# Kernel tuning notes

Measured on AMD Instinct MI355X. Metric: run time of the kernel, lower is better.

Reference implementation:

```python
import jax, jax.numpy as jnp
import numpy as np

EPS = 1e-6
CLASS_LAMBDA = 1.0
BBOX_LAMBDA = 1.0
IOU_LAMBDA = 1.0

B, Q, C1, T = 8, 900, 92, 1600  # batch, queries, num_classes+1, total targets


def _make_boxes(u):
    # turn uniform [.,4] noise into valid xyxy boxes in [0,1]
    xy = u[..., :2] * 0.7
    wh = u[..., 2:] * 0.3 + 0.01
    return jnp.concatenate([xy, xy + wh], axis=-1)


def setup_inputs() -> dict:
    key = jax.random.key(0)
    k1, k2, k3, k4 = jax.random.split(key, 4)
    pred_logits = jax.random.normal(k1, (B, Q, C1), dtype=jnp.float32)
    pred_bbox = _make_boxes(jax.random.uniform(k2, (B, Q, 4), dtype=jnp.float32))
    tgt_ids = jax.random.randint(k3, (T,), 0, 91, dtype=jnp.int32)
    tgt_bbox = _make_boxes(jax.random.uniform(k4, (T, 4), dtype=jnp.float32))
    return {"pred_logits": pred_logits, "pred_bbox": pred_bbox,
            "tgt_ids": tgt_ids, "tgt_bbox": tgt_bbox}


def _ciou_pairwise(b1, b2):
    # b1: [M,4], b2: [N,4] xyxy -> CIoU [M,N]
    b1 = b1[:, None, :]
    b2 = b2[None, :, :]
    x1 = jnp.maximum(b1[..., 0], b2[..., 0])
    y1 = jnp.maximum(b1[..., 1], b2[..., 1])
    x2 = jnp.minimum(b1[..., 2], b2[..., 2])
    y2 = jnp.minimum(b1[..., 3], b2[..., 3])
    inter = jnp.clip(x2 - x1, 0.0) * jnp.clip(y2 - y1, 0.0)
    w1 = b1[..., 2] - b1[..., 0]
    h1 = b1[..., 3] - b1[..., 1]
    w2 = b2[..., 2] - b2[..., 0]
    h2 = b2[..., 3] - b2[..., 1]
    union = w1 * h1 + w2 * h2 - inter
    iou = inter / (union + EPS)
    cw = jnp.maximum(b1[..., 2], b2[..., 2]) - jnp.minimum(b1[..., 0], b2[..., 0])
    ch = jnp.maximum(b1[..., 3], b2[..., 3]) - jnp.minimum(b1[..., 1], b2[..., 1])
    convex_diag_sq = cw ** 2 + ch ** 2
    center_dist_sq = ((b2[..., 0] + b2[..., 2] - b1[..., 0] - b1[..., 2]) ** 2
                      + (b2[..., 1] + b2[..., 3] - b1[..., 1] - b1[..., 3]) ** 2)
    dist_penalty = center_dist_sq / (convex_diag_sq + EPS) / 4.0
    v = (4.0 / jnp.pi ** 2) * (jnp.arctan(w2 / (h2 + EPS)) - jnp.arctan(w1 / (h1 + EPS))) ** 2
    alpha = jax.lax.stop_gradient(v / (1.0 + EPS - iou + v))  # torch no_grad
    return iou - dist_penalty - alpha * v


def reference(pred_logits, pred_bbox, tgt_ids, tgt_bbox):
    bsz, nq = pred_logits.shape[:2]
    out_prob = jax.nn.softmax(pred_logits.reshape(bsz * nq, -1), axis=-1)  # [BQ, C+1]
    out_bbox = pred_bbox.reshape(bsz * nq, 4)                              # [BQ, 4]
    cost_class = -out_prob[:, tgt_ids]                                     # [BQ, T]
    # L1 cdist
    cost_bbox = jnp.sum(jnp.abs(out_bbox[:, None, :] - tgt_bbox[None, :, :]), axis=-1)
    cost_iou = -_ciou_pairwise(out_bbox, tgt_bbox)                         # [BQ, T]
    cost = BBOX_LAMBDA * cost_bbox + CLASS_LAMBDA * cost_class + IOU_LAMBDA * cost_iou
    return cost.reshape(bsz, nq, -1)  # [B, Q, T]
```

## Files before the change

kernel.cpp:

```cpp
#include <hip/hip_runtime.h>
#include <math.h>

#define EPSF 1e-6f

constexpr int B_ = 8, Q_ = 900, C1_ = 92, T_ = 1600;
constexpr int NROW = B_ * Q_;
constexpr int PSTRIDE = 96;
constexpr int RPB = 16;
constexpr int TPB = 320;

__global__ __launch_bounds__(64) void precompute_kernel(
    const float* __restrict__ logits,
    const float* __restrict__ pbox,
    const float* __restrict__ tbox,
    float* __restrict__ probs,
    float* __restrict__ predd,
    float* __restrict__ tgtd)
{
    const int bid  = blockIdx.x;
    const int lane = threadIdx.x;

    if (bid < NROW) {
        const float* lrow = logits + (size_t)bid * C1_;
        float x0 = -INFINITY, x1 = -INFINITY;
        if (lane < C1_)      x0 = lrow[lane];
        if (lane + 64 < C1_) x1 = lrow[lane + 64];
        float m = fmaxf(x0, x1);
        #pragma unroll
        for (int off = 32; off; off >>= 1) m = fmaxf(m, __shfl_xor(m, off));
        float e0 = (lane < C1_)      ? __expf(x0 - m) : 0.0f;
        float e1 = (lane + 64 < C1_) ? __expf(x1 - m) : 0.0f;
        float s = e0 + e1;
        #pragma unroll
        for (int off = 32; off; off >>= 1) s += __shfl_xor(s, off);
        const float inv = 1.0f / s;
        float* prow = probs + (size_t)bid * PSTRIDE;
        if (lane < C1_)      prow[lane]      = e0 * inv;
        if (lane + 64 < C1_) prow[lane + 64] = e1 * inv;

        if (lane == 0) {
            const float bx1 = pbox[bid * 4 + 0];
            const float by1 = pbox[bid * 4 + 1];
            const float bx2 = pbox[bid * 4 + 2];
            const float by2 = pbox[bid * 4 + 3];
            const float w = bx2 - bx1, h = by2 - by1;
            float* d = predd + bid * 8;
            d[0] = bx1; d[1] = by1; d[2] = bx2; d[3] = by2;
            d[4] = w * h;
            d[5] = atanf(w / (h + EPSF));
            d[6] = bx1 + bx2;
            d[7] = by1 + by2;
        }
    } else {
        const int t = (bid - NROW) * 64 + lane;
        if (t < T_) {
            const float bx1 = tbox[t * 4 + 0];
            const float by1 = tbox[t * 4 + 1];
            const float bx2 = tbox[t * 4 + 2];
            const float by2 = tbox[t * 4 + 3];
            const float w = bx2 - bx1, h = by2 - by1;
            float* d = tgtd + t * 8;
            d[0] = bx1; d[1] = by1; d[2] = bx2; d[3] = by2;
            d[4] = w * h;
            d[5] = atanf(w / (h + EPSF));
            d[6] = bx1 + bx2;
            d[7] = by1 + by2;
        }
    }
}

__global__ __launch_bounds__(TPB) void cost_kernel(
    const float* __restrict__ probs,
    const float* __restrict__ predd,
    const float* __restrict__ tgtd,
    const int*   __restrict__ ids,
    float* __restrict__ out)
{
    __shared__ float sprobs[RPB * PSTRIDE];
    __shared__ float spredd[RPB * 8];

    const int tid  = threadIdx.x;
    const int t    = blockIdx.x * TPB + tid;
    const int row0 = blockIdx.y * RPB;

    {
        const float4* gp4 = (const float4*)(probs + (size_t)row0 * PSTRIDE);
        float4* sp4 = (float4*)sprobs;
        sp4[tid] = gp4[tid];
        if (tid < RPB * PSTRIDE / 4 - TPB)
            sp4[tid + TPB] = gp4[tid + TPB];
        const float4* gd4 = (const float4*)(predd + (size_t)row0 * 8);
        float4* sd4 = (float4*)spredd;
        if (tid < RPB * 8 / 4)
            sd4[tid] = gd4[tid];
    }

    const float4 ta = *(const float4*)(tgtd + (size_t)t * 8);
    const float4 tb = *(const float4*)(tgtd + (size_t)t * 8 + 4);
    const int id = ids[t];
    const float tx1 = ta.x, ty1 = ta.y, tx2 = ta.z, ty2 = ta.w;
    const float area2 = tb.x, atan2t = tb.y, sx2 = tb.z, sy2 = tb.w;

    __syncthreads();

    float* outp = out + (size_t)row0 * T_ + t;
    #pragma unroll 4
    for (int r = 0; r < RPB; ++r) {
        const float4 pa = *(const float4*)(spredd + r * 8);
        const float4 pb = *(const float4*)(spredd + r * 8 + 4);
        const float px1 = pa.x, py1 = pa.y, px2 = pa.z, py2 = pa.w;
        const float area1 = pb.x, atan1t = pb.y, sx1 = pb.z, sy1 = pb.w;

        const float prob = sprobs[r * PSTRIDE + id];

        const float ix1 = fmaxf(px1, tx1);
        const float iy1 = fmaxf(py1, ty1);
        const float ix2 = fminf(px2, tx2);
        const float iy2 = fminf(py2, ty2);
        const float inter = fmaxf(ix2 - ix1, 0.0f) * fmaxf(iy2 - iy1, 0.0f);
        const float uni = area1 + area2 - inter;
        const float iou = inter * __builtin_amdgcn_rcpf(uni + EPSF);

        const float cw = fmaxf(px2, tx2) - fminf(px1, tx1);
        const float ch = fmaxf(py2, ty2) - fminf(py1, ty1);
        const float diag = cw * cw + ch * ch;
        const float dx = sx2 - sx1, dy = sy2 - sy1;
        const float cdist = dx * dx + dy * dy;
        const float dist_pen = cdist * __builtin_amdgcn_rcpf(diag + EPSF) * 0.25f;

        const float dat = atan2t - atan1t;
        const float v = (4.0f / (float)(M_PI * M_PI)) * dat * dat;
        const float av = v * v * __builtin_amdgcn_rcpf(1.0f + EPSF - iou + v);

        const float ciou = iou - dist_pen - av;

        const float cost_bbox = fabsf(px1 - tx1) + fabsf(py1 - ty1) +
                                fabsf(px2 - tx2) + fabsf(py2 - ty2);

        __builtin_nontemporal_store(cost_bbox - prob - ciou, outp);
        outp += T_;
    }
}

extern "C" void kernel_launch(void* const* d_in, const int* in_sizes, int n_in,
                              void* d_out, int out_size, void* d_ws, size_t ws_size,
                              hipStream_t stream) {
    const float* logits = (const float*)d_in[0];
    const float* pbox   = (const float*)d_in[1];
    const int*   ids    = (const int*)d_in[2];
    const float* tbox   = (const float*)d_in[3];
    float* out = (float*)d_out;

    float* ws    = (float*)d_ws;
    float* probs = ws;
    float* predd = probs + (size_t)NROW * PSTRIDE;
    float* tgtd  = predd + (size_t)NROW * 8;

    const int nTgtBlocks = (T_ + 63) / 64;
    precompute_kernel<<<NROW + nTgtBlocks, 64, 0, stream>>>(
        logits, pbox, tbox, probs, predd, tgtd);

    cost_kernel<<<dim3(T_ / TPB, NROW / RPB), TPB, 0, stream>>>(
        probs, predd, tgtd, ids, out);
}
```

Baseline: 96.03 us.

## Fuse softmax and box precompute into the cost kernel, dropping the precompute launch

Removes the separate precompute kernel. Each cost block now loads its 16 raw logit rows into shared memory and runs the softmax there with per-wave shuffle reductions, computes the predicted-box derived values in shared memory, and computes target-box derived values, including the atan, per thread. This cuts a kernel launch and the workspace round trip through global memory. In exchange the softmax is recomputed once per column block (5x redundant), an extra barrier is added, and each thread evaluates an atan.

```diff
diff --git a/kernel.cpp b/kernel.cpp
--- a/kernel.cpp
+++ b/kernel.cpp
@@ -5,78 +5,18 @@
 
 constexpr int B_ = 8, Q_ = 900, C1_ = 92, T_ = 1600;
 constexpr int NROW = B_ * Q_;
-constexpr int PSTRIDE = 96;
 constexpr int RPB = 16;
 constexpr int TPB = 320;
+constexpr int LSTRIDE = 92;
 
-__global__ __launch_bounds__(64) void precompute_kernel(
+__global__ __launch_bounds__(TPB) void fused_cost_kernel(
     const float* __restrict__ logits,
     const float* __restrict__ pbox,
+    const int*   __restrict__ ids,
     const float* __restrict__ tbox,
-    float* __restrict__ probs,
-    float* __restrict__ predd,
-    float* __restrict__ tgtd)
-{
-    const int bid  = blockIdx.x;
-    const int lane = threadIdx.x;
-
-    if (bid < NROW) {
-        const float* lrow = logits + (size_t)bid * C1_;
-        float x0 = -INFINITY, x1 = -INFINITY;
-        if (lane < C1_)      x0 = lrow[lane];
-        if (lane + 64 < C1_) x1 = lrow[lane + 64];
-        float m = fmaxf(x0, x1);
-        #pragma unroll
-        for (int off = 32; off; off >>= 1) m = fmaxf(m, __shfl_xor(m, off));
-        float e0 = (lane < C1_)      ? __expf(x0 - m) : 0.0f;
-        float e1 = (lane + 64 < C1_) ? __expf(x1 - m) : 0.0f;
-        float s = e0 + e1;
-        #pragma unroll
-        for (int off = 32; off; off >>= 1) s += __shfl_xor(s, off);
-        const float inv = 1.0f / s;
-        float* prow = probs + (size_t)bid * PSTRIDE;
-        if (lane < C1_)      prow[lane]      = e0 * inv;
-        if (lane + 64 < C1_) prow[lane + 64] = e1 * inv;
-
-        if (lane == 0) {
-            const float bx1 = pbox[bid * 4 + 0];
-            const float by1 = pbox[bid * 4 + 1];
-            const float bx2 = pbox[bid * 4 + 2];
-            const float by2 = pbox[bid * 4 + 3];
-            const float w = bx2 - bx1, h = by2 - by1;
-            float* d = predd + bid * 8;
-            d[0] = bx1; d[1] = by1; d[2] = bx2; d[3] = by2;
-            d[4] = w * h;
-            d[5] = atanf(w / (h + EPSF));
-            d[6] = bx1 + bx2;
-            d[7] = by1 + by2;
-        }
-    } else {
-        const int t = (bid - NROW) * 64 + lane;
-        if (t < T_) {
-            const float bx1 = tbox[t * 4 + 0];
-            const float by1 = tbox[t * 4 + 1];
-            const float bx2 = tbox[t * 4 + 2];
-            const float by2 = tbox[t * 4 + 3];
-            const float w = bx2 - bx1, h = by2 - by1;
-            float* d = tgtd + t * 8;
-            d[0] = bx1; d[1] = by1; d[2] = bx2; d[3] = by2;
-            d[4] = w * h;
-            d[5] = atanf(w / (h + EPSF));
-            d[6] = bx1 + bx2;
-            d[7] = by1 + by2;
-        }
-    }
-}
-
-__global__ __launch_bounds__(TPB) void cost_kernel(
-    const float* __restrict__ probs,
-    const float* __restrict__ predd,
-    const float* __restrict__ tgtd,
-    const int*   __restrict__ ids,
     float* __restrict__ out)
 {
-    __shared__ float sprobs[RPB * PSTRIDE];
+    __shared__ float sprobs[RPB * LSTRIDE];
     __shared__ float spredd[RPB * 8];
 
     const int tid  = threadIdx.x;
@@ -84,22 +24,54 @@
     const int row0 = blockIdx.y * RPB;
 
     {
-        const float4* gp4 = (const float4*)(probs + (size_t)row0 * PSTRIDE);
-        float4* sp4 = (float4*)sprobs;
-        sp4[tid] = gp4[tid];
-        if (tid < RPB * PSTRIDE / 4 - TPB)
-            sp4[tid + TPB] = gp4[tid + TPB];
-        const float4* gd4 = (const float4*)(predd + (size_t)row0 * 8);
-        float4* sd4 = (float4*)spredd;
-        if (tid < RPB * 8 / 4)
-            sd4[tid] = gd4[tid];
+        const float4* gl4 = (const float4*)(logits + (size_t)row0 * C1_);
+        float4* sl4 = (float4*)sprobs;
+        sl4[tid] = gl4[tid];
+        if (tid < RPB * C1_ / 4 - TPB)
+            sl4[tid + TPB] = gl4[tid + TPB];
     }
 
-    const float4 ta = *(const float4*)(tgtd + (size_t)t * 8);
-    const float4 tb = *(const float4*)(tgtd + (size_t)t * 8 + 4);
+    const float4 tb4 = *(const float4*)(tbox + (size_t)t * 4);
     const int id = ids[t];
-    const float tx1 = ta.x, ty1 = ta.y, tx2 = ta.z, ty2 = ta.w;
-    const float area2 = tb.x, atan2t = tb.y, sx2 = tb.z, sy2 = tb.w;
+    const float tx1 = tb4.x, ty1 = tb4.y, tx2 = tb4.z, ty2 = tb4.w;
+    const float w2 = tx2 - tx1, h2 = ty2 - ty1;
+    const float area2  = w2 * h2;
+    const float atan2t = atanf(w2 / (h2 + EPSF));
+    const float sx2 = tx1 + tx2, sy2 = ty1 + ty2;
+
+    if (tid < RPB) {
+        const float4 pb4 = *(const float4*)(pbox + (size_t)(row0 + tid) * 4);
+        const float w = pb4.z - pb4.x, h = pb4.w - pb4.y;
+        float* d = spredd + tid * 8;
+        d[0] = pb4.x; d[1] = pb4.y; d[2] = pb4.z; d[3] = pb4.w;
+        d[4] = w * h;
+        d[5] = atanf(w / (h + EPSF));
+        d[6] = pb4.x + pb4.z;
+        d[7] = pb4.y + pb4.w;
+    }
+
+    __syncthreads();
+
+    {
+        const int wave = tid >> 6;
+        const int lane = tid & 63;
+        for (int r = wave; r < RPB; r += TPB / 64) {
+            float* row = sprobs + r * LSTRIDE;
+            const float x0 = row[lane];
+            const float x1 = (lane + 64 < C1_) ? row[lane + 64] : -INFINITY;
+            float m = fmaxf(x0, x1);
+            #pragma unroll
+            for (int off = 32; off; off >>= 1) m = fmaxf(m, __shfl_xor(m, off));
+            const float e0 = __expf(x0 - m);
+            const float e1 = (lane + 64 < C1_) ? __expf(x1 - m) : 0.0f;
+            float s = e0 + e1;
+            #pragma unroll
+            for (int off = 32; off; off >>= 1) s += __shfl_xor(s, off);
+            const float inv = 1.0f / s;
+            row[lane] = e0 * inv;
+            if (lane + 64 < C1_) row[lane + 64] = e1 * inv;
+        }
+    }
 
     __syncthreads();
 
@@ -111,7 +83,7 @@
         const float px1 = pa.x, py1 = pa.y, px2 = pa.z, py2 = pa.w;
         const float area1 = pb.x, atan1t = pb.y, sx1 = pb.z, sy1 = pb.w;
 
-        const float prob = sprobs[r * PSTRIDE + id];
+        const float prob = sprobs[r * LSTRIDE + id];
 
         const float ix1 = fmaxf(px1, tx1);
         const float iy1 = fmaxf(py1, ty1);
@@ -151,15 +123,6 @@
     const float* tbox   = (const float*)d_in[3];
     float* out = (float*)d_out;
 
-    float* ws    = (float*)d_ws;
-    float* probs = ws;
-    float* predd = probs + (size_t)NROW * PSTRIDE;
-    float* tgtd  = predd + (size_t)NROW * 8;
-
-    const int nTgtBlocks = (T_ + 63) / 64;
-    precompute_kernel<<<NROW + nTgtBlocks, 64, 0, stream>>>(
-        logits, pbox, tbox, probs, predd, tgtd);
-
-    cost_kernel<<<dim3(T_ / TPB, NROW / RPB), TPB, 0, stream>>>(
-        probs, predd, tgtd, ids, out);
+    fused_cost_kernel<<<dim3(T_ / TPB, NROW / RPB), TPB, 0, stream>>>(
+        logits, pbox, ids, tbox, out);
 }
```

Result: no change. 95.05 us (-1.0%).
